# Kernel tuning notes

Hardware: AMD Instinct MI355X
Metric: run time of the kernel (lower is better)

Reference implementation:

```python
import jax, jax.numpy as jnp
import numpy as np

NA = 10        # num_agents
P = 65536      # num_parallel envs
IN = 16        # input_size
DP = 2         # dim_p
E = 64         # embed_dim = hidden_dim // 2
H = 128        # h_dim


def _uniform(key, shape):
    # torch init: uniform(-stdv, stdv) with stdv = 1/sqrt(last_dim)
    stdv = 1.0 / np.sqrt(shape[-1])
    return jax.random.uniform(key, shape, jnp.float32, -stdv, stdv)


def setup_inputs() -> dict:
    key = jax.random.key(0)
    ks = jax.random.split(key, 8)
    inp = jax.random.normal(ks[0], (NA * P, IN), jnp.float32)
    W_enc = _uniform(ks[1], (IN - DP, E))
    b_enc = jnp.zeros((E,), jnp.float32)
    W_goal = _uniform(ks[2], (DP, E))
    b_goal = jnp.zeros((E,), jnp.float32)
    Wq = _uniform(ks[3], (E, E))   # n_heads=1, key_dim=val_dim=E
    Wk = _uniform(ks[4], (E, E))
    Wv = _uniform(ks[5], (E, E))
    Wo = _uniform(ks[6], (E, E))
    W_upd = _uniform(ks[7], (2 * E, E))
    b_upd = jnp.zeros((E,), jnp.float32)
    return dict(inp=inp, W_enc=W_enc, b_enc=b_enc, W_goal=W_goal, b_goal=b_goal,
                Wq=Wq, Wk=Wk, Wv=Wv, Wo=Wo, W_upd=W_upd, b_upd=b_upd)


def reference(inp, W_enc, b_enc, W_goal, b_goal, Wq, Wk, Wv, Wo, W_upd, b_upd):
    # split agent features / goal
    agent_inp = inp[:, :IN - DP]                     # (NA*P, 14)
    # goal: view(NA, P, DP).transpose(0,1)[:, 0, :] == first P rows' goal cols
    goal = inp[:P, IN - DP:]                         # (P, DP)

    # encoder: Linear + ReLU, then regroup agent-major -> (P, NA, E)
    h = jax.nn.relu(agent_inp @ W_enc + b_enc)
    h = h.reshape(NA, P, E).transpose(1, 0, 2)       # (P, NA, E)

    # single-head attention with custom mask (eye + first column blocked)
    scale = 1.0 / np.sqrt(E)
    Q = h @ Wq                                       # (P, NA, E)
    K = h @ Wk
    V = h @ Wv
    compat = jnp.einsum('bqd,bkd->bqk', Q, K) * scale  # (P, NA, NA)
    mask = jnp.eye(NA, dtype=bool) | (jnp.arange(NA)[None, :] == 0)
    compat = jnp.where(mask[None, :, :], -jnp.inf, compat)
    attn = jax.nn.softmax(compat, axis=-1)
    m = jnp.einsum('bqk,bkd->bqd', attn, V) @ Wo     # (P, NA, E)

    # update MLP on [h, m]
    h1 = jax.nn.relu(jnp.concatenate([h, m], axis=2) @ W_upd + b_upd)  # (P, NA, E)

    # second half: goal embedding for leader, leader's h for followers
    h2_leader = jax.nn.relu(goal @ W_goal + b_goal)[:, None, :]        # (P, 1, E)
    h2_followers = jnp.broadcast_to(h[:, :1, :], (P, NA - 1, E))        # (P, NA-1, E)
    h2 = jnp.concatenate([h2_leader, h2_followers], axis=1)            # (P, NA, E)

    hc = jnp.concatenate([h1, h2], axis=2)           # (P, NA, H)
    h_leader = hc[:, 0, :]                           # (P, H)
    h_followers = hc[:, 1:, :].transpose(1, 0, 2).reshape(-1, H)  # ((NA-1)*P, H)
    return (h_leader, h_followers)
```

## Files before the change

### kernel.cpp

```cpp
#include <hip/hip_runtime.h>
#include <math.h>

#define NAG 10
#define PP  65536
#define EE  64
#define INW 16
#define TP  4
#define RR  (TP*NAG)
#define SH  72
#define SX  40
#define SOT 132
#define NBLK 1024
#define NGRP (PP/TP)

typedef __attribute__((ext_vector_type(8))) short short8;
typedef __attribute__((ext_vector_type(4))) float f32x4;

__device__ __forceinline__ short f2bf(float x){
    unsigned u = __float_as_uint(x);
    u += 0x7FFF + ((u >> 16) & 1);
    return (short)(u >> 16);
}
__device__ __forceinline__ float bf2f(short s){
    return __uint_as_float(((unsigned)(unsigned short)s) << 16);
}

__global__ __launch_bounds__(256, 4) void mpnn_mfma2(
    const float* __restrict__ inp,
    const float* __restrict__ W_enc, const float* __restrict__ b_enc,
    const float* __restrict__ W_goal, const float* __restrict__ b_goal,
    const float* __restrict__ Wq, const float* __restrict__ Wk,
    const float* __restrict__ Wv, const float* __restrict__ Wo,
    const float* __restrict__ W_upd, const float* __restrict__ b_upd,
    float* __restrict__ out)
{
    __shared__ __align__(16) char pool[4 * 48 * SH * 2];
    __shared__ __align__(16) short Xs[48 * SX];
    __shared__ float attn_s[TP][NAG][12];
    __shared__ float goal_s[TP][2];

    short* const hs   = (short*)pool;
    short* const qsb  = hs  + 48*SH;
    short* const ksb  = qsb + 48*SH;
    short* const vsb  = ksb + 48*SH;
    float* const outt = (float*)pool;
    float* const Wc   = (float*)pool;

    const int tid  = threadIdx.x;
    const int w    = tid >> 6;
    const int l    = tid & 63;
    const int lrow = l & 15;
    const int lk   = l >> 4;
    const int col  = 16*w + lrow;

    for (int i = tid; i < EE*EE; i += 256) {
        const int k = i >> 6, n = i & 63;
        float s = 0.f;
        #pragma unroll 8
        for (int d = 0; d < EE; ++d)
            s = fmaf(Wo[k*EE + d], W_upd[(EE + d)*EE + n], s);
        Wc[i] = s;
    }
    __syncthreads();

    short8 fenc, fqw[2], fkw[2], fvw[2], fuw[2], fcw[2];
    #pragma unroll
    for (int j = 0; j < 8; ++j) {
        int k = lk*8 + j;
        fenc[j] = (k < 14) ? f2bf(W_enc[k*EE + col]) : (short)0;
    }
    #pragma unroll
    for (int ks = 0; ks < 2; ++ks) {
        #pragma unroll
        for (int j = 0; j < 8; ++j) {
            int k = 32*ks + lk*8 + j;
            fqw[ks][j] = f2bf(Wq[k*EE + col]);
            fkw[ks][j] = f2bf(Wk[k*EE + col]);
            fvw[ks][j] = f2bf(Wv[k*EE + col]);
            fuw[ks][j] = f2bf(W_upd[k*EE + col]);
            fcw[ks][j] = f2bf(Wc[k*EE + col]);
        }
    }
    const float bencv = b_enc[col];
    const float bupdv = b_upd[col];
    const float wg0 = W_goal[l], wg1 = W_goal[EE + l], bg = b_goal[l];

    for (int i = tid; i < 48*SX; i += 256) Xs[i] = 0;

    const bool hasx = tid < RR*4;
    const int  r_ = tid >> 2, q_ = tid & 3;
    const int  pl_ = r_ / NAG, a_ = r_ - pl_*NAG;
    const size_t xbase = (size_t)a_*PP*INW + (size_t)pl_*INW + (size_t)q_*4;
    float4 xin = {0,0,0,0};
    if (hasx) xin = *(const float4*)(inp + xbase + (size_t)blockIdx.x * (TP*INW));

    for (int g = blockIdx.x; g < NGRP; g += NBLK) {
        const int p0 = g * TP;
        __syncthreads();

        if (hasx) {
            short* xr = &Xs[r_*SX + q_*4];
            xr[0] = f2bf(xin.x); xr[1] = f2bf(xin.y);
            if (q_ == 3 && a_ == 0) {
                goal_s[pl_][0] = xin.z; goal_s[pl_][1] = xin.w;
            } else {
                xr[2] = f2bf(xin.z); xr[3] = f2bf(xin.w);
            }
        }
        __syncthreads();

        if (hasx && g + NBLK < NGRP)
            xin = *(const float4*)(inp + xbase + (size_t)(g + NBLK) * (TP*INW));

        const float h2l = fmaxf(fmaf(goal_s[w][0], wg0,
                           fmaf(goal_s[w][1], wg1, bg)), 0.f);

        #pragma unroll
        for (int rt = 0; rt < 3; ++rt) {
            const short8 a0 = *reinterpret_cast<const short8*>(&Xs[(16*rt + lrow)*SX + lk*8]);
            f32x4 acc = {0.f,0.f,0.f,0.f};
            acc = __builtin_amdgcn_mfma_f32_16x16x32_bf16(a0, fenc, acc, 0,0,0);
            #pragma unroll
            for (int j = 0; j < 4; ++j)
                hs[(16*rt + lk*4 + j)*SH + col] = f2bf(fmaxf(acc[j] + bencv, 0.f));
        }
        __syncthreads();

        #pragma unroll
        for (int rt = 0; rt < 3; ++rt) {
            const short8 a0 = *reinterpret_cast<const short8*>(&hs[(16*rt + lrow)*SH + lk*8]);
            const short8 a1 = *reinterpret_cast<const short8*>(&hs[(16*rt + lrow)*SH + 32 + lk*8]);
            f32x4 qa = {0.f,0.f,0.f,0.f}, ka = {0.f,0.f,0.f,0.f}, va = {0.f,0.f,0.f,0.f};
            qa = __builtin_amdgcn_mfma_f32_16x16x32_bf16(a0, fqw[0], qa, 0,0,0);
            qa = __builtin_amdgcn_mfma_f32_16x16x32_bf16(a1, fqw[1], qa, 0,0,0);
            ka = __builtin_amdgcn_mfma_f32_16x16x32_bf16(a0, fkw[0], ka, 0,0,0);
            ka = __builtin_amdgcn_mfma_f32_16x16x32_bf16(a1, fkw[1], ka, 0,0,0);
            va = __builtin_amdgcn_mfma_f32_16x16x32_bf16(a0, fvw[0], va, 0,0,0);
            va = __builtin_amdgcn_mfma_f32_16x16x32_bf16(a1, fvw[1], va, 0,0,0);
            #pragma unroll
            for (int j = 0; j < 4; ++j) {
                const int ro = (16*rt + lk*4 + j)*SH + col;
                qsb[ro] = f2bf(qa[j]);
                ksb[ro] = f2bf(ka[j]);
                vsb[ro] = f2bf(va[j]);
            }
        }
        const float h0 = bf2f(hs[(w*NAG)*SH + l]);
        __syncthreads();

        {
            const int r0 = w * NAG;
            for (int idx = l; idx < NAG*NAG; idx += 64) {
                const int q = idx / NAG, kk = idx - q*NAG;
                float c = -1e30f;
                if (kk != q && kk != 0) {
                    float s = 0.f;
                    #pragma unroll
                    for (int c8 = 0; c8 < 8; ++c8) {
                        const short8 qv = *reinterpret_cast<const short8*>(&qsb[(r0+q )*SH + c8*8]);
                        const short8 kv = *reinterpret_cast<const short8*>(&ksb[(r0+kk)*SH + c8*8]);
                        #pragma unroll
                        for (int i = 0; i < 8; ++i)
                            s = fmaf(bf2f(qv[i]), bf2f(kv[i]), s);
                    }
                    c = s * 0.125f;
                }
                attn_s[w][q][kk] = c;
            }
            if (l < NAG) {
                const int q = l;
                float mx = -1e30f;
                #pragma unroll
                for (int kk = 0; kk < NAG; ++kk) mx = fmaxf(mx, attn_s[w][q][kk]);
                float ex[NAG]; float sum = 0.f;
                #pragma unroll
                for (int kk = 0; kk < NAG; ++kk) { ex[kk] = __expf(attn_s[w][q][kk] - mx); sum += ex[kk]; }
                const float inv = 1.f / sum;
                #pragma unroll
                for (int kk = 0; kk < NAG; ++kk) attn_s[w][q][kk] = ex[kk] * inv;
            }
            float m[NAG];
            #pragma unroll
            for (int a = 0; a < NAG; ++a) m[a] = 0.f;
            #pragma unroll
            for (int kk = 0; kk < NAG; ++kk) {
                const float vk = bf2f(vsb[(r0+kk)*SH + l]);
                #pragma unroll
                for (int a = 0; a < NAG; ++a)
                    m[a] = fmaf(attn_s[w][a][kk], vk, m[a]);
            }
            #pragma unroll
            for (int a = 0; a < NAG; ++a) qsb[(r0+a)*SH + l] = f2bf(m[a]);
        }
        __syncthreads();

        f32x4 uacc[3];
        #pragma unroll
        for (int rt = 0; rt < 3; ++rt) {
            const short8 a0 = *reinterpret_cast<const short8*>(&hs [(16*rt + lrow)*SH + lk*8]);
            const short8 a1 = *reinterpret_cast<const short8*>(&hs [(16*rt + lrow)*SH + 32 + lk*8]);
            const short8 a2 = *reinterpret_cast<const short8*>(&qsb[(16*rt + lrow)*SH + lk*8]);
            const short8 a3 = *reinterpret_cast<const short8*>(&qsb[(16*rt + lrow)*SH + 32 + lk*8]);
            f32x4 ua = {0.f,0.f,0.f,0.f};
            ua = __builtin_amdgcn_mfma_f32_16x16x32_bf16(a0, fuw[0], ua, 0,0,0);
            ua = __builtin_amdgcn_mfma_f32_16x16x32_bf16(a1, fuw[1], ua, 0,0,0);
            ua = __builtin_amdgcn_mfma_f32_16x16x32_bf16(a2, fcw[0], ua, 0,0,0);
            ua = __builtin_amdgcn_mfma_f32_16x16x32_bf16(a3, fcw[1], ua, 0,0,0);
            uacc[rt] = ua;
        }
        __syncthreads();

        #pragma unroll
        for (int rt = 0; rt < 3; ++rt) {
            #pragma unroll
            for (int j = 0; j < 4; ++j) {
                const int r = 16*rt + lk*4 + j;
                if (r < RR) outt[r*SOT + col] = fmaxf(uacc[rt][j] + bupdv, 0.f);
            }
        }
        outt[(w*NAG)*SOT + 64 + l] = h2l;
        #pragma unroll
        for (int a = 1; a < NAG; ++a)
            outt[(w*NAG + a)*SOT + 64 + l] = h0;
        __syncthreads();

        float* __restrict__ outF = out + (size_t)PP*128;
        #pragma unroll
        for (int it = 0; it < 5; ++it) {
            const int flat   = it*256 + tid;
            const int a      = flat >> 7;
            const int within = flat & 127;
            const int pl     = within >> 5;
            const int j4     = within & 31;
            const float4 v = *(const float4*)&outt[(pl*NAG + a)*SOT + j4*4];
            float* dst = (a == 0)
                ? (out  + ((size_t)(p0 + pl))*128 + j4*4)
                : (outF + ((size_t)(a-1)*PP + (size_t)(p0 + pl))*128 + j4*4);
            *(float4*)dst = v;
        }
    }
}

extern "C" void kernel_launch(void* const* d_in, const int* in_sizes, int n_in,
                              void* d_out, int out_size, void* d_ws, size_t ws_size,
                              hipStream_t stream) {
    const float* inp    = (const float*)d_in[0];
    const float* W_enc  = (const float*)d_in[1];
    const float* b_enc  = (const float*)d_in[2];
    const float* W_goal = (const float*)d_in[3];
    const float* b_goal = (const float*)d_in[4];
    const float* Wq     = (const float*)d_in[5];
    const float* Wk     = (const float*)d_in[6];
    const float* Wv     = (const float*)d_in[7];
    const float* Wo     = (const float*)d_in[8];
    const float* W_upd  = (const float*)d_in[9];
    const float* b_upd  = (const float*)d_in[10];

    hipLaunchKernelGGL(mpnn_mfma2, dim3(NBLK), dim3(256), 0, stream,
                       inp, W_enc, b_enc, W_goal, b_goal,
                       Wq, Wk, Wv, Wo, W_upd, b_upd, (float*)d_out);
}
```

Baseline: 274.1 us.

## Compute attention scores with MFMA, add nontemporal I/O, reuse h fragments

Attention scores QK^T are now computed with two bf16 MFMA instructions per wave instead of scalar dot products, and the softmax is done in registers with cross-lane shuffles. The loads of h fragments from the Q/K/V stage are kept in registers and reused in the update GEMM. Input loads and output stores use nontemporal hints, and the bf16 rounding is simplified from round-to-nearest-even to round-half-up. The attn-times-V step reads attention weights as float2. Together these aim to cut the ALU and LDS work in the attention stage and reduce cache pollution from streaming traffic. The cost is extra register pressure and slightly different rounding.

```diff
diff --git a/kernel.cpp b/kernel.cpp
--- a/kernel.cpp
+++ b/kernel.cpp
@@ -18,14 +18,13 @@
 
 __device__ __forceinline__ short f2bf(float x){
     unsigned u = __float_as_uint(x);
-    u += 0x7FFF + ((u >> 16) & 1);
-    return (short)(u >> 16);
+    return (short)((u + 0x8000u) >> 16);
 }
 __device__ __forceinline__ float bf2f(short s){
     return __uint_as_float(((unsigned)(unsigned short)s) << 16);
 }
 
-__global__ __launch_bounds__(256, 4) void mpnn_mfma2(
+__global__ __launch_bounds__(256, 4) void mpnn_mfma3(
     const float* __restrict__ inp,
     const float* __restrict__ W_enc, const float* __restrict__ b_enc,
     const float* __restrict__ W_goal, const float* __restrict__ b_goal,
@@ -36,7 +35,7 @@
 {
     __shared__ __align__(16) char pool[4 * 48 * SH * 2];
     __shared__ __align__(16) short Xs[48 * SX];
-    __shared__ float attn_s[TP][NAG][12];
+    __shared__ __align__(16) float attn_s[TP][NAG][12];
     __shared__ float goal_s[TP][2];
 
     short* const hs   = (short*)pool;
@@ -91,8 +90,9 @@
     const int  r_ = tid >> 2, q_ = tid & 3;
     const int  pl_ = r_ / NAG, a_ = r_ - pl_*NAG;
     const size_t xbase = (size_t)a_*PP*INW + (size_t)pl_*INW + (size_t)q_*4;
-    float4 xin = {0,0,0,0};
-    if (hasx) xin = *(const float4*)(inp + xbase + (size_t)blockIdx.x * (TP*INW));
+    f32x4 xin = {0.f,0.f,0.f,0.f};
+    if (hasx) xin = __builtin_nontemporal_load(
+        (const f32x4*)(inp + xbase + (size_t)blockIdx.x * (TP*INW)));
 
     for (int g = blockIdx.x; g < NGRP; g += NBLK) {
         const int p0 = g * TP;
@@ -100,17 +100,18 @@
 
         if (hasx) {
             short* xr = &Xs[r_*SX + q_*4];
-            xr[0] = f2bf(xin.x); xr[1] = f2bf(xin.y);
+            xr[0] = f2bf(xin[0]); xr[1] = f2bf(xin[1]);
             if (q_ == 3 && a_ == 0) {
-                goal_s[pl_][0] = xin.z; goal_s[pl_][1] = xin.w;
+                goal_s[pl_][0] = xin[2]; goal_s[pl_][1] = xin[3];
             } else {
-                xr[2] = f2bf(xin.z); xr[3] = f2bf(xin.w);
+                xr[2] = f2bf(xin[2]); xr[3] = f2bf(xin[3]);
             }
         }
         __syncthreads();
 
         if (hasx && g + NBLK < NGRP)
-            xin = *(const float4*)(inp + xbase + (size_t)(g + NBLK) * (TP*INW));
+            xin = __builtin_nontemporal_load(
+                (const f32x4*)(inp + xbase + (size_t)(g + NBLK) * (TP*INW)));
 
         const float h2l = fmaxf(fmaf(goal_s[w][0], wg0,
                            fmaf(goal_s[w][1], wg1, bg)), 0.f);
@@ -126,17 +127,18 @@
         }
         __syncthreads();
 
-        #pragma unroll
-        for (int rt = 0; rt < 3; ++rt) {
-            const short8 a0 = *reinterpret_cast<const short8*>(&hs[(16*rt + lrow)*SH + lk*8]);
-            const short8 a1 = *reinterpret_cast<const short8*>(&hs[(16*rt + lrow)*SH + 32 + lk*8]);
+        short8 hA0[3], hA1[3];
+        #pragma unroll
+        for (int rt = 0; rt < 3; ++rt) {
+            hA0[rt] = *reinterpret_cast<const short8*>(&hs[(16*rt + lrow)*SH + lk*8]);
+            hA1[rt] = *reinterpret_cast<const short8*>(&hs[(16*rt + lrow)*SH + 32 + lk*8]);
             f32x4 qa = {0.f,0.f,0.f,0.f}, ka = {0.f,0.f,0.f,0.f}, va = {0.f,0.f,0.f,0.f};
-            qa = __builtin_amdgcn_mfma_f32_16x16x32_bf16(a0, fqw[0], qa, 0,0,0);
-            qa = __builtin_amdgcn_mfma_f32_16x16x32_bf16(a1, fqw[1], qa, 0,0,0);
-            ka = __builtin_amdgcn_mfma_f32_16x16x32_bf16(a0, fkw[0], ka, 0,0,0);
-            ka = __builtin_amdgcn_mfma_f32_16x16x32_bf16(a1, fkw[1], ka, 0,0,0);
-            va = __builtin_amdgcn_mfma_f32_16x16x32_bf16(a0, fvw[0], va, 0,0,0);
-            va = __builtin_amdgcn_mfma_f32_16x16x32_bf16(a1, fvw[1], va, 0,0,0);
+            qa = __builtin_amdgcn_mfma_f32_16x16x32_bf16(hA0[rt], fqw[0], qa, 0,0,0);
+            qa = __builtin_amdgcn_mfma_f32_16x16x32_bf16(hA1[rt], fqw[1], qa, 0,0,0);
+            ka = __builtin_amdgcn_mfma_f32_16x16x32_bf16(hA0[rt], fkw[0], ka, 0,0,0);
+            ka = __builtin_amdgcn_mfma_f32_16x16x32_bf16(hA1[rt], fkw[1], ka, 0,0,0);
+            va = __builtin_amdgcn_mfma_f32_16x16x32_bf16(hA0[rt], fvw[0], va, 0,0,0);
+            va = __builtin_amdgcn_mfma_f32_16x16x32_bf16(hA1[rt], fvw[1], va, 0,0,0);
             #pragma unroll
             for (int j = 0; j < 4; ++j) {
                 const int ro = (16*rt + lk*4 + j)*SH + col;
@@ -150,62 +152,65 @@
 
         {
             const int r0 = w * NAG;
-            for (int idx = l; idx < NAG*NAG; idx += 64) {
-                const int q = idx / NAG, kk = idx - q*NAG;
-                float c = -1e30f;
-                if (kk != q && kk != 0) {
-                    float s = 0.f;
-                    #pragma unroll
-                    for (int c8 = 0; c8 < 8; ++c8) {
-                        const short8 qv = *reinterpret_cast<const short8*>(&qsb[(r0+q )*SH + c8*8]);
-                        const short8 kv = *reinterpret_cast<const short8*>(&ksb[(r0+kk)*SH + c8*8]);
-                        #pragma unroll
-                        for (int i = 0; i < 8; ++i)
-                            s = fmaf(bf2f(qv[i]), bf2f(kv[i]), s);
-                    }
-                    c = s * 0.125f;
+            const short8 aK0 = *reinterpret_cast<const short8*>(&ksb[(r0+lrow)*SH + lk*8]);
+            const short8 aK1 = *reinterpret_cast<const short8*>(&ksb[(r0+lrow)*SH + 32 + lk*8]);
+            const short8 aQ0 = *reinterpret_cast<const short8*>(&qsb[(r0+lrow)*SH + lk*8]);
+            const short8 aQ1 = *reinterpret_cast<const short8*>(&qsb[(r0+lrow)*SH + 32 + lk*8]);
+            f32x4 st = {0.f,0.f,0.f,0.f};
+            st = __builtin_amdgcn_mfma_f32_16x16x32_bf16(aK0, aQ0, st, 0,0,0);
+            st = __builtin_amdgcn_mfma_f32_16x16x32_bf16(aK1, aQ1, st, 0,0,0);
+            const int q = lrow;
+            float c[4]; float mx4 = -1e30f;
+            #pragma unroll
+            for (int j = 0; j < 4; ++j) {
+                const int k = lk*4 + j;
+                const bool valid = (q < NAG) && (k < NAG) && (k != q) && (k != 0);
+                c[j] = valid ? st[j] * 0.125f : -1e30f;
+                mx4 = fmaxf(mx4, c[j]);
+            }
+            float mx = fmaxf(mx4, __shfl_xor(mx4, 16, 64));
+            mx = fmaxf(mx, __shfl_xor(mx, 32, 64));
+            float e[4], s4 = 0.f;
+            #pragma unroll
+            for (int j = 0; j < 4; ++j) { e[j] = __expf(c[j] - mx); s4 += e[j]; }
+            float s = s4;
+            s += __shfl_xor(s, 16, 64);
+            s += __shfl_xor(s, 32, 64);
+            const float inv = 1.f / s;
+            if (q < NAG) {
+                #pragma unroll
+                for (int j = 0; j < 4; ++j) {
+                    const int k = lk*4 + j;
+                    if (k < NAG) attn_s[w][q][k] = e[j] * inv;
                 }
-                attn_s[w][q][kk] = c;
-            }
-            if (l < NAG) {
-                const int q = l;
-                float mx = -1e30f;
+            }
+
+            float vv[NAG];
+            #pragma unroll
+            for (int kk = 0; kk < NAG; ++kk) vv[kk] = bf2f(vsb[(r0+kk)*SH + l]);
+            #pragma unroll
+            for (int a = 0; a < NAG; ++a) {
+                float m = 0.f;
                 #pragma unroll
-                for (int kk = 0; kk < NAG; ++kk) mx = fmaxf(mx, attn_s[w][q][kk]);
-                float ex[NAG]; float sum = 0.f;
-                #pragma unroll
-                for (int kk = 0; kk < NAG; ++kk) { ex[kk] = __expf(attn_s[w][q][kk] - mx); sum += ex[kk]; }
-                const float inv = 1.f / sum;
-                #pragma unroll
-                for (int kk = 0; kk < NAG; ++kk) attn_s[w][q][kk] = ex[kk] * inv;
-            }
-            float m[NAG];
-            #pragma unroll
-            for (int a = 0; a < NAG; ++a) m[a] = 0.f;
-            #pragma unroll
-            for (int kk = 0; kk < NAG; ++kk) {
-                const float vk = bf2f(vsb[(r0+kk)*SH + l]);
-                #pragma unroll
-                for (int a = 0; a < NAG; ++a)
-                    m[a] = fmaf(attn_s[w][a][kk], vk, m[a]);
-            }
-            #pragma unroll
-            for (int a = 0; a < NAG; ++a) qsb[(r0+a)*SH + l] = f2bf(m[a]);
+                for (int t = 0; t < 5; ++t) {
+                    const float2 pv = *reinterpret_cast<const float2*>(&attn_s[w][a][2*t]);
+                    m = fmaf(pv.x, vv[2*t], fmaf(pv.y, vv[2*t+1], m));
+                }
+                qsb[(r0+a)*SH + l] = f2bf(m);
+            }
         }
         __syncthreads();
 
         f32x4 uacc[3];
         #pragma unroll
         for (int rt = 0; rt < 3; ++rt) {
-            const short8 a0 = *reinterpret_cast<const short8*>(&hs [(16*rt + lrow)*SH + lk*8]);
-            const short8 a1 = *reinterpret_cast<const short8*>(&hs [(16*rt + lrow)*SH + 32 + lk*8]);
             const short8 a2 = *reinterpret_cast<const short8*>(&qsb[(16*rt + lrow)*SH + lk*8]);
             const short8 a3 = *reinterpret_cast<const short8*>(&qsb[(16*rt + lrow)*SH + 32 + lk*8]);
             f32x4 ua = {0.f,0.f,0.f,0.f};
-            ua = __builtin_amdgcn_mfma_f32_16x16x32_bf16(a0, fuw[0], ua, 0,0,0);
-            ua = __builtin_amdgcn_mfma_f32_16x16x32_bf16(a1, fuw[1], ua, 0,0,0);
-            ua = __builtin_amdgcn_mfma_f32_16x16x32_bf16(a2, fcw[0], ua, 0,0,0);
-            ua = __builtin_amdgcn_mfma_f32_16x16x32_bf16(a3, fcw[1], ua, 0,0,0);
+            ua = __builtin_amdgcn_mfma_f32_16x16x32_bf16(hA0[rt], fuw[0], ua, 0,0,0);
+            ua = __builtin_amdgcn_mfma_f32_16x16x32_bf16(hA1[rt], fuw[1], ua, 0,0,0);
+            ua = __builtin_amdgcn_mfma_f32_16x16x32_bf16(a2,      fcw[0], ua, 0,0,0);
+            ua = __builtin_amdgcn_mfma_f32_16x16x32_bf16(a3,      fcw[1], ua, 0,0,0);
             uacc[rt] = ua;
         }
         __syncthreads();
@@ -232,11 +237,11 @@
             const int within = flat & 127;
             const int pl     = within >> 5;
             const int j4     = within & 31;
-            const float4 v = *(const float4*)&outt[(pl*NAG + a)*SOT + j4*4];
+            const f32x4 v = *reinterpret_cast<const f32x4*>(&outt[(pl*NAG + a)*SOT + j4*4]);
             float* dst = (a == 0)
                 ? (out  + ((size_t)(p0 + pl))*128 + j4*4)
                 : (outF + ((size_t)(a-1)*PP + (size_t)(p0 + pl))*128 + j4*4);
-            *(float4*)dst = v;
+            __builtin_nontemporal_store(v, (f32x4*)dst);
         }
     }
 }
@@ -256,7 +261,7 @@
     const float* W_upd  = (const float*)d_in[9];
     const float* b_upd  = (const float*)d_in[10];
 
-    hipLaunchKernelGGL(mpnn_mfma2, dim3(NBLK), dim3(256), 0, stream,
+    hipLaunchKernelGGL(mpnn_mfma3, dim3(NBLK), dim3(256), 0, stream,
                        inp, W_enc, b_enc, W_goal, b_goal,
                        Wq, Wk, Wv, Wo, W_upd, b_upd, (float*)d_out);
 }
```

New measurement: 255.0 us. 1.07x faster.
